# Performance work log

Measured on AMD Instinct MI355X. Metric: run time of the kernel, lower is better.

## Reference

```python
import jax, jax.numpy as jnp
import numpy as np

DIM = 128      # channels C
HEADS = 4
HD = DIM // HEADS  # head_dim = 32
N = 128        # window tokens = 2*8*8
BW = 2048      # B_ = batch * num_windows
NP = 256       # sp_mask partitions
NW = 256       # shift-mask windows
TABLE = 675    # (2*2-1)*(2*8-1)*(2*8-1)
SCALE = HD ** -0.5


def setup_inputs() -> dict:
    key = jax.random.key(0)
    ks = jax.random.split(key, 8)
    x = jax.random.normal(ks[0], (BW, N, DIM), jnp.float32)
    rpi = jax.random.randint(ks[1], (N, N), 0, TABLE, dtype=jnp.int32)
    mask = jax.random.normal(ks[2], (NW, N, N), jnp.float32)
    sp_mask = jax.random.normal(ks[3], (NP, N, N), jnp.float32)
    w_qkv = jax.random.normal(ks[4], (3 * DIM, DIM), jnp.float32) * 0.02
    b_qkv = jnp.zeros((3 * DIM,), jnp.float32)
    bias_table = jax.random.normal(ks[5], (TABLE, HEADS), jnp.float32) * 0.02
    w_proj = jax.random.normal(ks[6], (DIM, DIM), jnp.float32) * 0.02
    b_proj = jnp.zeros((DIM,), jnp.float32)
    return {"x": x, "rpi": rpi, "mask": mask, "sp_mask": sp_mask,
            "w_qkv": w_qkv, "b_qkv": b_qkv, "bias_table": bias_table,
            "w_proj": w_proj, "b_proj": b_proj}


def reference(x, rpi, mask, sp_mask, w_qkv, b_qkv, bias_table, w_proj, b_proj):
    B_, Nn, C = x.shape
    # qkv projection -> (B_, N, 3, H, hd)
    qkv = (x @ w_qkv.T + b_qkv).reshape(B_, Nn, 3, HEADS, HD)
    q = qkv[:, :, 0].transpose(0, 2, 1, 3) * SCALE  # (B_, H, N, hd)
    k = qkv[:, :, 1].transpose(0, 2, 1, 3)
    v = qkv[:, :, 2].transpose(0, 2, 1, 3)
    attn = jnp.einsum('bhnd,bhmd->bhnm', q, k)  # (B_, H, N, N)
    # gathered relative position bias: (N, N, H) -> (H, N, N)
    rpb = bias_table[rpi].transpose(2, 0, 1)
    attn = attn + rpb[None]
    # additive sparse mask, broadcast over B_//nP groups and heads
    attn = (attn.reshape(B_ // NP, NP, HEADS, Nn, Nn)
            + sp_mask[None, :, None]).reshape(B_, HEADS, Nn, Nn)
    # additive shift mask, broadcast over B_//nW groups and heads
    attn = (attn.reshape(B_ // NW, NW, HEADS, Nn, Nn)
            + mask[None, :, None]).reshape(B_, HEADS, Nn, Nn)
    attn = jax.nn.softmax(attn, axis=-1)
    out = jnp.einsum('bhnm,bhmd->bnhd', attn, v).reshape(B_, Nn, C)
    return out @ w_proj.T + b_proj
```

## Files before the change

### kernel.cpp

```cpp
#include <hip/hip_runtime.h>

typedef short v8s __attribute__((ext_vector_type(8)));
typedef float v4f __attribute__((ext_vector_type(4)));

#define MFMA16(a, b, c) __builtin_amdgcn_mfma_f32_16x16x32_bf16(a, b, c, 0, 0, 0)

__device__ __forceinline__ unsigned short f2b(float f) {
  union { float f; unsigned int i; } v;
  v.f = f;
  unsigned int x = v.i;
  return (unsigned short)((x + 0x7fffu + ((x >> 16) & 1u)) >> 16);
}
__device__ __forceinline__ unsigned int cvtpk(float lo, float hi) {
  unsigned int r;
  asm("v_cvt_pk_bf16_f32 %0, %1, %2" : "=v"(r) : "v"(lo), "v"(hi));
  return r;
}

#define SCALE 0.17677669529663687f
#define LOG2E 1.4426950408889634f
#define QSCALE (SCALE * LOG2E)

#define WS_RPB 16777216
#define WS_WQH 17039360
#define WS_WPH 17137664

__global__ __launch_bounds__(256)
void build_pre(const float* __restrict__ mask, const float* __restrict__ sp,
               const int* __restrict__ rpi, const float* __restrict__ btab,
               const float* __restrict__ wq, const float* __restrict__ wp,
               float* __restrict__ msum, float* __restrict__ rpb,
               unsigned short* __restrict__ wqh, unsigned short* __restrict__ wph) {
  const int wgrp = blockIdx.x >> 3, slab = blockIdx.x & 7, tid = threadIdx.x;
  const size_t base = (size_t)wgrp * 16384 + slab * 2048;
  const float* mk = mask + base;
  const float* sk = sp + base;
  float* ot = msum + base;
  for (int it = 0; it < 2; ++it) {
    int i = (tid + 256 * it) * 4;
    float4 a = *(const float4*)(mk + i);
    float4 b = *(const float4*)(sk + i);
    float4 s;
    s.x = (a.x + b.x) * LOG2E; s.y = (a.y + b.y) * LOG2E;
    s.z = (a.z + b.z) * LOG2E; s.w = (a.w + b.w) * LOG2E;
    *(float4*)(ot + i) = s;
  }
  int e = blockIdx.x * 256 + tid;
  if (e < 65536) {
    int hh = e >> 14, r = e & 16383;
    rpb[e] = btab[rpi[r] * 4 + hh] * LOG2E;
  }
  if (blockIdx.x >= 256 && blockIdx.x < 512) {
    int w = (blockIdx.x - 256) * 256 + tid;
    if (w < 384 * 128) wqh[w] = f2b(wq[w]);
    else wph[w - 384 * 128] = f2b(wp[w - 384 * 128]);
  }
}

__global__ __launch_bounds__(1024, 4)
void attn_fused(const float* __restrict__ xg,
                const unsigned short* __restrict__ wqh,
                const float* __restrict__ bq,
                const float* __restrict__ msum,
                const float* __restrict__ rpb,
                const unsigned short* __restrict__ wph,
                const float* __restrict__ bpj,
                float* __restrict__ out) {
  __shared__ alignas(16) unsigned char smem[110592];
  unsigned short* xs = (unsigned short*)smem;
  unsigned short* os = (unsigned short*)smem;

  const int tid = threadIdx.x;
  const int wid = tid >> 6;
  const int s = wid & 3;
  const int h = wid >> 2;
  const int lane = tid & 63;
  const int qd = lane >> 4;
  const int t16 = lane & 15;

  const int idx = blockIdx.x;
  const int wgrp = idx >> 3;
  const int b = (idx & 7) * 256 + wgrp;

  unsigned short* kss = (unsigned short*)(smem + 34816 + h * 10240);
  unsigned short* vs  = (unsigned short*)(smem + 75776 + h * 8704);

  {
    const float* src = xg + (size_t)b * 16384;
    for (int it = 0; it < 2; ++it) {
      int gl = tid + 1024 * it;
      int row = gl >> 4, g = gl & 15;
      const float4* s4 = (const float4*)(src + row * 128 + g * 8);
      float4 a = s4[0], c = s4[1];
      union { int4 v; unsigned int d[4]; } pk;
      pk.d[0] = cvtpk(a.x, a.y); pk.d[1] = cvtpk(a.z, a.w);
      pk.d[2] = cvtpk(c.x, c.y); pk.d[3] = cvtpk(c.z, c.w);
      *(int4*)(xs + row * 128 + ((g ^ (row & 15)) << 3)) = pk.v;
    }
  }
  __syncthreads();

  v8s bx[2][4];
  for (int nt = 0; nt < 2; ++nt)
    for (int ks = 0; ks < 4; ++ks) {
      int n = 32 * s + nt * 16 + t16;
      int g = ks * 4 + qd;
      bx[nt][ks] = *(const v8s*)(xs + n * 128 + ((g ^ (n & 15)) << 3));
    }

  v4f accqk[4][2];
  for (int jt = 0; jt < 4; ++jt)
    for (int nt = 0; nt < 2; ++nt) accqk[jt][nt] = v4f{0.f, 0.f, 0.f, 0.f};
  for (int jt = 0; jt < 4; ++jt) {
    int wbase = (jt < 2) ? (h * 32 + jt * 16) : (128 + h * 32 + (jt - 2) * 16);
    for (int ks = 0; ks < 4; ++ks) {
      v8s a = *(const v8s*)(wqh + (wbase + t16) * 128 + ks * 32 + 8 * qd);
      for (int nt = 0; nt < 2; ++nt)
        accqk[jt][nt] = MFMA16(a, bx[nt][ks], accqk[jt][nt]);
    }
  }
  v4f accv[2][2];
  for (int rt = 0; rt < 2; ++rt)
    for (int ct = 0; ct < 2; ++ct) accv[rt][ct] = v4f{0.f, 0.f, 0.f, 0.f};
  for (int ct = 0; ct < 2; ++ct)
    for (int ks = 0; ks < 4; ++ks) {
      v8s bw = *(const v8s*)(wqh + (256 + h * 32 + ct * 16 + t16) * 128 + ks * 32 + 8 * qd);
      for (int rt = 0; rt < 2; ++rt)
        accv[rt][ct] = MFMA16(bx[rt][ks], bw, accv[rt][ct]);
    }

  for (int jt = 2; jt < 4; ++jt)
    for (int nt = 0; nt < 2; ++nt) {
      int n = 32 * s + nt * 16 + t16;
      int bb = 128 + h * 32 + (jt - 2) * 16 + 4 * qd;
      uint2 pk;
      pk.x = cvtpk(accqk[jt][nt][0] + bq[bb + 0], accqk[jt][nt][1] + bq[bb + 1]);
      pk.y = cvtpk(accqk[jt][nt][2] + bq[bb + 2], accqk[jt][nt][3] + bq[bb + 3]);
      *(uint2*)(kss + n * 40 + (jt - 2) * 16 + 4 * qd) = pk;
    }
  for (int ct = 0; ct < 2; ++ct) {
    int d = ct * 16 + t16;
    float bv = bq[256 + h * 32 + d];
    for (int rt = 0; rt < 2; ++rt) {
      uint2 pk;
      pk.x = cvtpk(accv[rt][ct][0] + bv, accv[rt][ct][1] + bv);
      pk.y = cvtpk(accv[rt][ct][2] + bv, accv[rt][ct][3] + bv);
      *(uint2*)(vs + d * 136 + 32 * s + rt * 16 + 4 * qd) = pk;
    }
  }

  unsigned int qpk[2][2][2];
  for (int jt = 0; jt < 2; ++jt)
    for (int nt = 0; nt < 2; ++nt) {
      int bb = h * 32 + jt * 16 + 4 * qd;
      float v0 = (accqk[jt][nt][0] + bq[bb + 0]) * QSCALE;
      float v1 = (accqk[jt][nt][1] + bq[bb + 1]) * QSCALE;
      float v2 = (accqk[jt][nt][2] + bq[bb + 2]) * QSCALE;
      float v3 = (accqk[jt][nt][3] + bq[bb + 3]) * QSCALE;
      qpk[jt][nt][0] = cvtpk(v0, v1);
      qpk[jt][nt][1] = cvtpk(v2, v3);
    }
  const int srcA = ((qd & 1) << 5) + t16;
  const bool hiq = qd >= 2;
  v8s aq[2];
  for (int rt = 0; rt < 2; ++rt) {
    union { v8s v; unsigned int d[4]; } u;
    unsigned int a0 = __shfl((int)qpk[0][rt][0], srcA, 64);
    unsigned int b0 = __shfl((int)qpk[1][rt][0], srcA, 64);
    unsigned int a1 = __shfl((int)qpk[0][rt][1], srcA, 64);
    unsigned int b1 = __shfl((int)qpk[1][rt][1], srcA, 64);
    unsigned int a2 = __shfl((int)qpk[0][rt][0], srcA + 16, 64);
    unsigned int b2 = __shfl((int)qpk[1][rt][0], srcA + 16, 64);
    unsigned int a3 = __shfl((int)qpk[0][rt][1], srcA + 16, 64);
    unsigned int b3 = __shfl((int)qpk[1][rt][1], srcA + 16, 64);
    u.d[0] = hiq ? b0 : a0;
    u.d[1] = hiq ? b1 : a1;
    u.d[2] = hiq ? b2 : a2;
    u.d[3] = hiq ? b3 : a3;
    aq[rt] = u.v;
  }
  __syncthreads();

  v4f sa[2][8];
  const v4f zero4 = {0.f, 0.f, 0.f, 0.f};
  for (int ct = 0; ct < 8; ++ct) {
    v8s bk = *(const v8s*)(kss + (ct * 16 + t16) * 40 + 8 * qd);
    for (int nt = 0; nt < 2; ++nt)
      sa[nt][ct] = MFMA16(bk, aq[nt], zero4);
  }
  {
    const float* mt = msum + (size_t)wgrp * 16384;
    const float* rb = rpb + (size_t)h * 16384;
    for (int nt = 0; nt < 2; ++nt) {
      int n = 32 * s + nt * 16 + t16;
      const float* pm = mt + n * 128;
      const float* pr = rb + n * 128;
      for (int ct = 0; ct < 8; ++ct) {
        float4 b1 = *(const float4*)(pm + ct * 16 + 4 * qd);
        float4 b2 = *(const float4*)(pr + ct * 16 + 4 * qd);
        sa[nt][ct][0] += b1.x + b2.x;
        sa[nt][ct][1] += b1.y + b2.y;
        sa[nt][ct][2] += b1.z + b2.z;
        sa[nt][ct][3] += b1.w + b2.w;
      }
    }
  }
  float pinv[2];
  for (int nt = 0; nt < 2; ++nt) {
    for (int ct = 0; ct < 8; ++ct)
      for (int r = 0; r < 4; ++r)
        sa[nt][ct][r] = exp2f(sa[nt][ct][r]);
    float s0 = 0.f;
    for (int ct = 0; ct < 8; ++ct)
      for (int r = 0; r < 4; ++r) s0 += sa[nt][ct][r];
    s0 += __shfl_xor(s0, 16);
    s0 += __shfl_xor(s0, 32);
    pinv[nt] = 1.0f / s0;
  }

  v8s av[2][4];
  for (int rt = 0; rt < 2; ++rt)
    for (int ks = 0; ks < 4; ++ks)
      av[rt][ks] = *(const v8s*)(vs + (rt * 16 + t16) * 136 + ks * 32 + 8 * qd);

  const int srcP0 = ((qd & 1) << 5) + t16;
  const bool hip2 = qd >= 2;
  for (int nt = 0; nt < 2; ++nt) {
    unsigned int pkd[8][2];
    for (int ct = 0; ct < 8; ++ct) {
      pkd[ct][0] = cvtpk(sa[nt][ct][0], sa[nt][ct][1]);
      pkd[ct][1] = cvtpk(sa[nt][ct][2], sa[nt][ct][3]);
    }
    v8s bp[4];
    for (int ks = 0; ks < 4; ++ks) {
      union { v8s v; unsigned int d[4]; } u;
      unsigned int a0 = __shfl((int)pkd[2 * ks][0], srcP0, 64);
      unsigned int b0 = __shfl((int)pkd[2 * ks + 1][0], srcP0, 64);
      unsigned int a1 = __shfl((int)pkd[2 * ks][1], srcP0, 64);
      unsigned int b1 = __shfl((int)pkd[2 * ks + 1][1], srcP0, 64);
      unsigned int a2 = __shfl((int)pkd[2 * ks][0], srcP0 + 16, 64);
      unsigned int b2 = __shfl((int)pkd[2 * ks + 1][0], srcP0 + 16, 64);
      unsigned int a3 = __shfl((int)pkd[2 * ks][1], srcP0 + 16, 64);
      unsigned int b3 = __shfl((int)pkd[2 * ks + 1][1], srcP0 + 16, 64);
      u.d[0] = hip2 ? b0 : a0;
      u.d[1] = hip2 ? b1 : a1;
      u.d[2] = hip2 ? b2 : a2;
      u.d[3] = hip2 ? b3 : a3;
      bp[ks] = u.v;
    }
    v4f oa[2] = {zero4, zero4};
    for (int ks = 0; ks < 4; ++ks)
      for (int rt = 0; rt < 2; ++rt)
        oa[rt] = MFMA16(av[rt][ks], bp[ks], oa[rt]);
    int n = 32 * s + nt * 16 + t16;
    float sv = pinv[nt];
    for (int rt = 0; rt < 2; ++rt) {
      uint2 pk;
      pk.x = cvtpk(oa[rt][0] * sv, oa[rt][1] * sv);
      pk.y = cvtpk(oa[rt][2] * sv, oa[rt][3] * sv);
      *(uint2*)(os + n * 136 + h * 32 + rt * 16 + 4 * qd) = pk;
    }
  }
  __syncthreads();

  {
    const int tn = wid >> 1;
    const int rh = wid & 1;
    v8s ao[4];
    for (int ks = 0; ks < 4; ++ks)
      ao[ks] = *(const v8s*)(os + (tn * 16 + t16) * 136 + ks * 32 + 8 * qd);
    const size_t rowb = ((size_t)b * 128 + tn * 16 + t16) * 128;
    for (int rt0 = 0; rt0 < 4; ++rt0) {
      int rt = rh * 4 + rt0;
      v4f acc = zero4;
      for (int ks = 0; ks < 4; ++ks) {
        v8s a = *(const v8s*)(wph + (rt * 16 + t16) * 128 + ks * 32 + 8 * qd);
        acc = MFMA16(a, ao[ks], acc);
      }
      float4 bj = *(const float4*)(bpj + rt * 16 + 4 * qd);
      float4 pk;
      pk.x = acc[0] + bj.x;
      pk.y = acc[1] + bj.y;
      pk.z = acc[2] + bj.z;
      pk.w = acc[3] + bj.w;
      *(float4*)(out + rowb + rt * 16 + 4 * qd) = pk;
    }
  }
}

extern "C" void kernel_launch(void* const* d_in, const int* in_sizes, int n_in,
                              void* d_out, int out_size, void* d_ws, size_t ws_size,
                              hipStream_t stream) {
  (void)in_sizes; (void)n_in; (void)out_size; (void)ws_size;
  const float* xg   = (const float*)d_in[0];
  const int*   rpi  = (const int*)d_in[1];
  const float* mask = (const float*)d_in[2];
  const float* sp   = (const float*)d_in[3];
  const float* wq   = (const float*)d_in[4];
  const float* bq   = (const float*)d_in[5];
  const float* btab = (const float*)d_in[6];
  const float* wp   = (const float*)d_in[7];
  const float* bpj  = (const float*)d_in[8];
  float* out = (float*)d_out;

  float* msum = (float*)d_ws;
  float* rpb  = (float*)((char*)d_ws + WS_RPB);
  unsigned short* wqh = (unsigned short*)((char*)d_ws + WS_WQH);
  unsigned short* wph = (unsigned short*)((char*)d_ws + WS_WPH);

  build_pre<<<2048, 256, 0, stream>>>(mask, sp, rpi, btab, wq, wp,
                                      msum, rpb, wqh, wph);
  attn_fused<<<2048, 1024, 0, stream>>>(xg, wqh, bq, msum, rpb, wph, bpj, out);
}
```

Measured before the change: 547.1 us.

## Make attention kernel persistent per mask group with async x prefetch into LDS

```diff
diff --git a/kernel.cpp b/kernel.cpp
--- a/kernel.cpp
+++ b/kernel.cpp
@@ -24,6 +24,10 @@
 #define WS_RPB 16777216
 #define WS_WQH 17039360
 #define WS_WPH 17137664
+
+#define LDS_O 65536
+#define LDS_V 100352
+#define LDS_TOTAL 135168
 
 __global__ __launch_bounds__(256)
 void build_pre(const float* __restrict__ mask, const float* __restrict__ sp,
@@ -57,6 +61,19 @@
   }
 }
 
+__device__ __forceinline__ void stage_issue(const float* __restrict__ xb,
+                                            unsigned char* smem, int wid, int lane) {
+  for (int it = 0; it < 4; ++it) {
+    int p = wid * 256 + it * 64 + lane;
+    int row = p >> 5, g = p & 31;
+    const float* src = xb + row * 128 + ((g ^ (row & 31)) << 2);
+    unsigned char* dst = smem + (size_t)(wid * 256 + it * 64) * 16;
+    __builtin_amdgcn_global_load_lds(
+        (const __attribute__((address_space(1))) unsigned int*)src,
+        (__attribute__((address_space(3))) unsigned int*)dst, 16, 0, 0);
+  }
+}
+
 __global__ __launch_bounds__(1024, 4)
 void attn_fused(const float* __restrict__ xg,
                 const unsigned short* __restrict__ wqh,
@@ -66,9 +83,8 @@
                 const unsigned short* __restrict__ wph,
                 const float* __restrict__ bpj,
                 float* __restrict__ out) {
-  __shared__ alignas(16) unsigned char smem[110592];
-  unsigned short* xs = (unsigned short*)smem;
-  unsigned short* os = (unsigned short*)smem;
+  __shared__ alignas(16) unsigned char smem[LDS_TOTAL];
+  unsigned short* os = (unsigned short*)(smem + LDS_O);
 
   const int tid = threadIdx.x;
   const int wid = tid >> 6;
@@ -78,119 +94,114 @@
   const int qd = lane >> 4;
   const int t16 = lane & 15;
 
-  const int idx = blockIdx.x;
-  const int wgrp = idx >> 3;
-  const int b = (idx & 7) * 256 + wgrp;
-
-  unsigned short* kss = (unsigned short*)(smem + 34816 + h * 10240);
-  unsigned short* vs  = (unsigned short*)(smem + 75776 + h * 8704);
-
-  {
-    const float* src = xg + (size_t)b * 16384;
-    for (int it = 0; it < 2; ++it) {
-      int gl = tid + 1024 * it;
-      int row = gl >> 4, g = gl & 15;
-      const float4* s4 = (const float4*)(src + row * 128 + g * 8);
-      float4 a = s4[0], c = s4[1];
-      union { int4 v; unsigned int d[4]; } pk;
-      pk.d[0] = cvtpk(a.x, a.y); pk.d[1] = cvtpk(a.z, a.w);
-      pk.d[2] = cvtpk(c.x, c.y); pk.d[3] = cvtpk(c.z, c.w);
-      *(int4*)(xs + row * 128 + ((g ^ (row & 15)) << 3)) = pk.v;
-    }
-  }
-  __syncthreads();
-
-  v8s bx[2][4];
-  for (int nt = 0; nt < 2; ++nt)
-    for (int ks = 0; ks < 4; ++ks) {
-      int n = 32 * s + nt * 16 + t16;
-      int g = ks * 4 + qd;
-      bx[nt][ks] = *(const v8s*)(xs + n * 128 + ((g ^ (n & 15)) << 3));
-    }
-
-  v4f accqk[4][2];
-  for (int jt = 0; jt < 4; ++jt)
-    for (int nt = 0; nt < 2; ++nt) accqk[jt][nt] = v4f{0.f, 0.f, 0.f, 0.f};
-  for (int jt = 0; jt < 4; ++jt) {
-    int wbase = (jt < 2) ? (h * 32 + jt * 16) : (128 + h * 32 + (jt - 2) * 16);
-    for (int ks = 0; ks < 4; ++ks) {
-      v8s a = *(const v8s*)(wqh + (wbase + t16) * 128 + ks * 32 + 8 * qd);
+  const int wgrp = blockIdx.x;
+  unsigned short* kss = (unsigned short*)(smem + h * 10240);
+  unsigned short* vs  = (unsigned short*)(smem + LDS_V + h * 8704);
+  const float* mt = msum + (size_t)wgrp * 16384;
+  const float* rb = rpb + (size_t)h * 16384;
+  const v4f zero4 = {0.f, 0.f, 0.f, 0.f};
+
+  stage_issue(xg + (size_t)wgrp * 16384, smem, wid, lane);
+
+#pragma unroll 1
+  for (int bgrp = 0; bgrp < 8; ++bgrp) {
+    const int b = bgrp * 256 + wgrp;
+
+    __syncthreads();
+
+    v8s bx[2][4];
+    for (int nt = 0; nt < 2; ++nt)
+      for (int ks = 0; ks < 4; ++ks) {
+        int n = 32 * s + nt * 16 + t16;
+        int ga = ks * 8 + 2 * qd;
+        float4 flo = *(const float4*)(smem + ((n * 32 + (ga ^ (n & 31))) << 4));
+        float4 fhi = *(const float4*)(smem + ((n * 32 + ((ga + 1) ^ (n & 31))) << 4));
+        union { v8s v; unsigned int d[4]; } r;
+        r.d[0] = cvtpk(flo.x, flo.y); r.d[1] = cvtpk(flo.z, flo.w);
+        r.d[2] = cvtpk(fhi.x, fhi.y); r.d[3] = cvtpk(fhi.z, fhi.w);
+        bx[nt][ks] = r.v;
+      }
+    __syncthreads();
+
+    v4f accqk[4][2];
+    for (int jt = 0; jt < 4; ++jt)
+      for (int nt = 0; nt < 2; ++nt) accqk[jt][nt] = zero4;
+    for (int jt = 0; jt < 4; ++jt) {
+      int wbase = (jt < 2) ? (h * 32 + jt * 16) : (128 + h * 32 + (jt - 2) * 16);
+      for (int ks = 0; ks < 4; ++ks) {
+        v8s a = *(const v8s*)(wqh + (wbase + t16) * 128 + ks * 32 + 8 * qd);
+        for (int nt = 0; nt < 2; ++nt)
+          accqk[jt][nt] = MFMA16(a, bx[nt][ks], accqk[jt][nt]);
+      }
+    }
+    v4f accv[2][2];
+    for (int rt = 0; rt < 2; ++rt)
+      for (int ct = 0; ct < 2; ++ct) accv[rt][ct] = zero4;
+    for (int ct = 0; ct < 2; ++ct)
+      for (int ks = 0; ks < 4; ++ks) {
+        v8s bw = *(const v8s*)(wqh + (256 + h * 32 + ct * 16 + t16) * 128 + ks * 32 + 8 * qd);
+        for (int rt = 0; rt < 2; ++rt)
+          accv[rt][ct] = MFMA16(bx[rt][ks], bw, accv[rt][ct]);
+      }
+
+    for (int jt = 2; jt < 4; ++jt)
+      for (int nt = 0; nt < 2; ++nt) {
+        int n = 32 * s + nt * 16 + t16;
+        int bb = 128 + h * 32 + (jt - 2) * 16 + 4 * qd;
+        uint2 pk;
+        pk.x = cvtpk(accqk[jt][nt][0] + bq[bb + 0], accqk[jt][nt][1] + bq[bb + 1]);
+        pk.y = cvtpk(accqk[jt][nt][2] + bq[bb + 2], accqk[jt][nt][3] + bq[bb + 3]);
+        *(uint2*)(kss + n * 40 + (jt - 2) * 16 + 4 * qd) = pk;
+      }
+    for (int ct = 0; ct < 2; ++ct) {
+      int d = ct * 16 + t16;
+      float bv = bq[256 + h * 32 + d];
+      for (int rt = 0; rt < 2; ++rt) {
+        uint2 pk;
+        pk.x = cvtpk(accv[rt][ct][0] + bv, accv[rt][ct][1] + bv);
+        pk.y = cvtpk(accv[rt][ct][2] + bv, accv[rt][ct][3] + bv);
+        *(uint2*)(vs + d * 136 + 32 * s + rt * 16 + 4 * qd) = pk;
+      }
+    }
+
+    unsigned int qpk[2][2][2];
+    for (int jt = 0; jt < 2; ++jt)
+      for (int nt = 0; nt < 2; ++nt) {
+        int bb = h * 32 + jt * 16 + 4 * qd;
+        float v0 = (accqk[jt][nt][0] + bq[bb + 0]) * QSCALE;
+        float v1 = (accqk[jt][nt][1] + bq[bb + 1]) * QSCALE;
+        float v2 = (accqk[jt][nt][2] + bq[bb + 2]) * QSCALE;
+        float v3 = (accqk[jt][nt][3] + bq[bb + 3]) * QSCALE;
+        qpk[jt][nt][0] = cvtpk(v0, v1);
+        qpk[jt][nt][1] = cvtpk(v2, v3);
+      }
+    const int srcA = ((qd & 1) << 5) + t16;
+    const bool hiq = qd >= 2;
+    v8s aq[2];
+    for (int rt = 0; rt < 2; ++rt) {
+      union { v8s v; unsigned int d[4]; } u;
+      unsigned int a0 = __shfl((int)qpk[0][rt][0], srcA, 64);
+      unsigned int b0 = __shfl((int)qpk[1][rt][0], srcA, 64);
+      unsigned int a1 = __shfl((int)qpk[0][rt][1], srcA, 64);
+      unsigned int b1 = __shfl((int)qpk[1][rt][1], srcA, 64);
+      unsigned int a2 = __shfl((int)qpk[0][rt][0], srcA + 16, 64);
+      unsigned int b2 = __shfl((int)qpk[1][rt][0], srcA + 16, 64);
+      unsigned int a3 = __shfl((int)qpk[0][rt][1], srcA + 16, 64);
+      unsigned int b3 = __shfl((int)qpk[1][rt][1], srcA + 16, 64);
+      u.d[0] = hiq ? b0 : a0;
+      u.d[1] = hiq ? b1 : a1;
+      u.d[2] = hiq ? b2 : a2;
+      u.d[3] = hiq ? b3 : a3;
+      aq[rt] = u.v;
+    }
+    __syncthreads();
+
+    v4f sa[2][8];
+    for (int ct = 0; ct < 8; ++ct) {
+      v8s bk = *(const v8s*)(kss + (ct * 16 + t16) * 40 + 8 * qd);
       for (int nt = 0; nt < 2; ++nt)
-        accqk[jt][nt] = MFMA16(a, bx[nt][ks], accqk[jt][nt]);
-    }
-  }
-  v4f accv[2][2];
-  for (int rt = 0; rt < 2; ++rt)
-    for (int ct = 0; ct < 2; ++ct) accv[rt][ct] = v4f{0.f, 0.f, 0.f, 0.f};
-  for (int ct = 0; ct < 2; ++ct)
-    for (int ks = 0; ks < 4; ++ks) {
-      v8s bw = *(const v8s*)(wqh + (256 + h * 32 + ct * 16 + t16) * 128 + ks * 32 + 8 * qd);
-      for (int rt = 0; rt < 2; ++rt)
-        accv[rt][ct] = MFMA16(bx[rt][ks], bw, accv[rt][ct]);
-    }
-
-  for (int jt = 2; jt < 4; ++jt)
-    for (int nt = 0; nt < 2; ++nt) {
-      int n = 32 * s + nt * 16 + t16;
-      int bb = 128 + h * 32 + (jt - 2) * 16 + 4 * qd;
-      uint2 pk;
-      pk.x = cvtpk(accqk[jt][nt][0] + bq[bb + 0], accqk[jt][nt][1] + bq[bb + 1]);
-      pk.y = cvtpk(accqk[jt][nt][2] + bq[bb + 2], accqk[jt][nt][3] + bq[bb + 3]);
-      *(uint2*)(kss + n * 40 + (jt - 2) * 16 + 4 * qd) = pk;
-    }
-  for (int ct = 0; ct < 2; ++ct) {
-    int d = ct * 16 + t16;
-    float bv = bq[256 + h * 32 + d];
-    for (int rt = 0; rt < 2; ++rt) {
-      uint2 pk;
-      pk.x = cvtpk(accv[rt][ct][0] + bv, accv[rt][ct][1] + bv);
-      pk.y = cvtpk(accv[rt][ct][2] + bv, accv[rt][ct][3] + bv);
-      *(uint2*)(vs + d * 136 + 32 * s + rt * 16 + 4 * qd) = pk;
-    }
-  }
-
-  unsigned int qpk[2][2][2];
-  for (int jt = 0; jt < 2; ++jt)
-    for (int nt = 0; nt < 2; ++nt) {
-      int bb = h * 32 + jt * 16 + 4 * qd;
-      float v0 = (accqk[jt][nt][0] + bq[bb + 0]) * QSCALE;
-      float v1 = (accqk[jt][nt][1] + bq[bb + 1]) * QSCALE;
-      float v2 = (accqk[jt][nt][2] + bq[bb + 2]) * QSCALE;
-      float v3 = (accqk[jt][nt][3] + bq[bb + 3]) * QSCALE;
-      qpk[jt][nt][0] = cvtpk(v0, v1);
-      qpk[jt][nt][1] = cvtpk(v2, v3);
-    }
-  const int srcA = ((qd & 1) << 5) + t16;
-  const bool hiq = qd >= 2;
-  v8s aq[2];
-  for (int rt = 0; rt < 2; ++rt) {
-    union { v8s v; unsigned int d[4]; } u;
-    unsigned int a0 = __shfl((int)qpk[0][rt][0], srcA, 64);
-    unsigned int b0 = __shfl((int)qpk[1][rt][0], srcA, 64);
-    unsigned int a1 = __shfl((int)qpk[0][rt][1], srcA, 64);
-    unsigned int b1 = __shfl((int)qpk[1][rt][1], srcA, 64);
-    unsigned int a2 = __shfl((int)qpk[0][rt][0], srcA + 16, 64);
-    unsigned int b2 = __shfl((int)qpk[1][rt][0], srcA + 16, 64);
-    unsigned int a3 = __shfl((int)qpk[0][rt][1], srcA + 16, 64);
-    unsigned int b3 = __shfl((int)qpk[1][rt][1], srcA + 16, 64);
-    u.d[0] = hiq ? b0 : a0;
-    u.d[1] = hiq ? b1 : a1;
-    u.d[2] = hiq ? b2 : a2;
-    u.d[3] = hiq ? b3 : a3;
-    aq[rt] = u.v;
-  }
-  __syncthreads();
-
-  v4f sa[2][8];
-  const v4f zero4 = {0.f, 0.f, 0.f, 0.f};
-  for (int ct = 0; ct < 8; ++ct) {
-    v8s bk = *(const v8s*)(kss + (ct * 16 + t16) * 40 + 8 * qd);
-    for (int nt = 0; nt < 2; ++nt)
-      sa[nt][ct] = MFMA16(bk, aq[nt], zero4);
-  }
-  {
-    const float* mt = msum + (size_t)wgrp * 16384;
-    const float* rb = rpb + (size_t)h * 16384;
+        sa[nt][ct] = MFMA16(bk, aq[nt], zero4);
+    }
     for (int nt = 0; nt < 2; ++nt) {
       int n = 32 * s + nt * 16 + t16;
       const float* pm = mt + n * 128;
@@ -204,86 +215,89 @@
         sa[nt][ct][3] += b1.w + b2.w;
       }
     }
-  }
-  float pinv[2];
-  for (int nt = 0; nt < 2; ++nt) {
-    for (int ct = 0; ct < 8; ++ct)
-      for (int r = 0; r < 4; ++r)
-        sa[nt][ct][r] = exp2f(sa[nt][ct][r]);
-    float s0 = 0.f;
-    for (int ct = 0; ct < 8; ++ct)
-      for (int r = 0; r < 4; ++r) s0 += sa[nt][ct][r];
-    s0 += __shfl_xor(s0, 16);
-    s0 += __shfl_xor(s0, 32);
-    pinv[nt] = 1.0f / s0;
-  }
-
-  v8s av[2][4];
-  for (int rt = 0; rt < 2; ++rt)
-    for (int ks = 0; ks < 4; ++ks)
-      av[rt][ks] = *(const v8s*)(vs + (rt * 16 + t16) * 136 + ks * 32 + 8 * qd);
-
-  const int srcP0 = ((qd & 1) << 5) + t16;
-  const bool hip2 = qd >= 2;
-  for (int nt = 0; nt < 2; ++nt) {
-    unsigned int pkd[8][2];
-    for (int ct = 0; ct < 8; ++ct) {
-      pkd[ct][0] = cvtpk(sa[nt][ct][0], sa[nt][ct][1]);
-      pkd[ct][1] = cvtpk(sa[nt][ct][2], sa[nt][ct][3]);
-    }
-    v8s bp[4];
-    for (int ks = 0; ks < 4; ++ks) {
-      union { v8s v; unsigned int d[4]; } u;
-      unsigned int a0 = __shfl((int)pkd[2 * ks][0], srcP0, 64);
-      unsigned int b0 = __shfl((int)pkd[2 * ks + 1][0], srcP0, 64);
-      unsigned int a1 = __shfl((int)pkd[2 * ks][1], srcP0, 64);
-      unsigned int b1 = __shfl((int)pkd[2 * ks + 1][1], srcP0, 64);
-      unsigned int a2 = __shfl((int)pkd[2 * ks][0], srcP0 + 16, 64);
-      unsigned int b2 = __shfl((int)pkd[2 * ks + 1][0], srcP0 + 16, 64);
-      unsigned int a3 = __shfl((int)pkd[2 * ks][1], srcP0 + 16, 64);
-      unsigned int b3 = __shfl((int)pkd[2 * ks + 1][1], srcP0 + 16, 64);
-      u.d[0] = hip2 ? b0 : a0;
-      u.d[1] = hip2 ? b1 : a1;
-      u.d[2] = hip2 ? b2 : a2;
-      u.d[3] = hip2 ? b3 : a3;
-      bp[ks] = u.v;
-    }
-    v4f oa[2] = {zero4, zero4};
-    for (int ks = 0; ks < 4; ++ks)
-      for (int rt = 0; rt < 2; ++rt)
-        oa[rt] = MFMA16(av[rt][ks], bp[ks], oa[rt]);
-    int n = 32 * s + nt * 16 + t16;
-    float sv = pinv[nt];
-    for (int rt = 0; rt < 2; ++rt) {
-      uint2 pk;
-      pk.x = cvtpk(oa[rt][0] * sv, oa[rt][1] * sv);
-      pk.y = cvtpk(oa[rt][2] * sv, oa[rt][3] * sv);
-      *(uint2*)(os + n * 136 + h * 32 + rt * 16 + 4 * qd) = pk;
-    }
-  }
-  __syncthreads();
-
-  {
-    const int tn = wid >> 1;
-    const int rh = wid & 1;
-    v8s ao[4];
-    for (int ks = 0; ks < 4; ++ks)
-      ao[ks] = *(const v8s*)(os + (tn * 16 + t16) * 136 + ks * 32 + 8 * qd);
-    const size_t rowb = ((size_t)b * 128 + tn * 16 + t16) * 128;
-    for (int rt0 = 0; rt0 < 4; ++rt0) {
-      int rt = rh * 4 + rt0;
-      v4f acc = zero4;
+    float pinv[2];
+    for (int nt = 0; nt < 2; ++nt) {
+      for (int ct = 0; ct < 8; ++ct)
+        for (int r = 0; r < 4; ++r)
+          sa[nt][ct][r] = exp2f(sa[nt][ct][r]);
+      float s0 = 0.f;
+      for (int ct = 0; ct < 8; ++ct)
+        for (int r = 0; r < 4; ++r) s0 += sa[nt][ct][r];
+      s0 += __shfl_xor(s0, 16);
+      s0 += __shfl_xor(s0, 32);
+      pinv[nt] = 1.0f / s0;
+    }
+
+    v8s av[2][4];
+    for (int rt = 0; rt < 2; ++rt)
+      for (int ks = 0; ks < 4; ++ks)
+        av[rt][ks] = *(const v8s*)(vs + (rt * 16 + t16) * 136 + ks * 32 + 8 * qd);
+
+    const int srcP0 = ((qd & 1) << 5) + t16;
+    const bool hip2 = qd >= 2;
+    for (int nt = 0; nt < 2; ++nt) {
+      unsigned int pkd[8][2];
+      for (int ct = 0; ct < 8; ++ct) {
+        pkd[ct][0] = cvtpk(sa[nt][ct][0], sa[nt][ct][1]);
+        pkd[ct][1] = cvtpk(sa[nt][ct][2], sa[nt][ct][3]);
+      }
+      v8s bp[4];
       for (int ks = 0; ks < 4; ++ks) {
-        v8s a = *(const v8s*)(wph + (rt * 16 + t16) * 128 + ks * 32 + 8 * qd);
-        acc = MFMA16(a, ao[ks], acc);
-      }
-      float4 bj = *(const float4*)(bpj + rt * 16 + 4 * qd);
-      float4 pk;
-      pk.x = acc[0] + bj.x;
-      pk.y = acc[1] + bj.y;
-      pk.z = acc[2] + bj.z;
-      pk.w = acc[3] + bj.w;
-      *(float4*)(out + rowb + rt * 16 + 4 * qd) = pk;
+        union { v8s v; unsigned int d[4]; } u;
+        unsigned int a0 = __shfl((int)pkd[2 * ks][0], srcP0, 64);
+        unsigned int b0 = __shfl((int)pkd[2 * ks + 1][0], srcP0, 64);
+        unsigned int a1 = __shfl((int)pkd[2 * ks][1], srcP0, 64);
+        unsigned int b1 = __shfl((int)pkd[2 * ks + 1][1], srcP0, 64);
+        unsigned int a2 = __shfl((int)pkd[2 * ks][0], srcP0 + 16, 64);
+        unsigned int b2 = __shfl((int)pkd[2 * ks + 1][0], srcP0 + 16, 64);
+        unsigned int a3 = __shfl((int)pkd[2 * ks][1], srcP0 + 16, 64);
+        unsigned int b3 = __shfl((int)pkd[2 * ks + 1][1], srcP0 + 16, 64);
+        u.d[0] = hip2 ? b0 : a0;
+        u.d[1] = hip2 ? b1 : a1;
+        u.d[2] = hip2 ? b2 : a2;
+        u.d[3] = hip2 ? b3 : a3;
+        bp[ks] = u.v;
+      }
+      v4f oa[2] = {zero4, zero4};
+      for (int ks = 0; ks < 4; ++ks)
+        for (int rt = 0; rt < 2; ++rt)
+          oa[rt] = MFMA16(av[rt][ks], bp[ks], oa[rt]);
+      int n = 32 * s + nt * 16 + t16;
+      float sv = pinv[nt];
+      for (int rt = 0; rt < 2; ++rt) {
+        uint2 pk;
+        pk.x = cvtpk(oa[rt][0] * sv, oa[rt][1] * sv);
+        pk.y = cvtpk(oa[rt][2] * sv, oa[rt][3] * sv);
+        *(uint2*)(os + n * 136 + h * 32 + rt * 16 + 4 * qd) = pk;
+      }
+    }
+    __syncthreads();
+
+    if (bgrp < 7)
+      stage_issue(xg + (size_t)((bgrp + 1) * 256 + wgrp) * 16384, smem, wid, lane);
+
+    {
+      const int tn = wid >> 1;
+      const int rh = wid & 1;
+      v8s ao[4];
+      for (int ks = 0; ks < 4; ++ks)
+        ao[ks] = *(const v8s*)(os + (tn * 16 + t16) * 136 + ks * 32 + 8 * qd);
+      const size_t rowb = ((size_t)b * 128 + tn * 16 + t16) * 128;
+      for (int rt0 = 0; rt0 < 4; ++rt0) {
+        int rt = rh * 4 + rt0;
+        v4f acc = zero4;
+        for (int ks = 0; ks < 4; ++ks) {
+          v8s a = *(const v8s*)(wph + (rt * 16 + t16) * 128 + ks * 32 + 8 * qd);
+          acc = MFMA16(a, ao[ks], acc);
+        }
+        float4 bj = *(const float4*)(bpj + rt * 16 + 4 * qd);
+        float4 pk;
+        pk.x = acc[0] + bj.x;
+        pk.y = acc[1] + bj.y;
+        pk.z = acc[2] + bj.z;
+        pk.w = acc[3] + bj.w;
+        *(float4*)(out + rowb + rt * 16 + 4 * qd) = pk;
+      }
     }
   }
 }
@@ -310,5 +324,5 @@
 
   build_pre<<<2048, 256, 0, stream>>>(mask, sp, rpi, btab, wq, wp,
                                       msum, rpb, wqh, wph);
-  attn_fused<<<2048, 1024, 0, stream>>>(xg, wqh, bq, msum, rpb, wph, bpj, out);
-}
+  attn_fused<<<256, 1024, 0, stream>>>(xg, wqh, bq, msum, rpb, wph, bpj, out);
+}
```

Result: slower. 682.6 us (+24.8%).
